# Performance work log

Measured on AMD Instinct MI355X. Metric: run time of the kernel, lower is better.

The kernel has to match this reference:

```python
import jax, jax.numpy as jnp
import numpy as np

BLOCK_SIZE = 16
NVFP4_LEVELS = np.array([0.0, 0.5, 1.0, 1.5, 2.0, 3.0, 4.0, 6.0], dtype=np.float32)


def quantize_to_nvfp4(x, block_size=BLOCK_SIZE):
    """NVFP4 fake-quant: per-16-element block, scale = amax/6, round |x| to nearest level."""
    levels = jnp.asarray(NVFP4_LEVELS, dtype=x.dtype)
    orig_shape = x.shape
    xf = x.reshape(-1, block_size)                                   # [nblk, 16]
    amax = jnp.clip(jnp.max(jnp.abs(xf), axis=-1, keepdims=True), 1e-12)
    scale = amax / 6.0                                               # [nblk, 1]
    x_norm = jnp.abs(xf) / scale                                     # in [0, 6]
    idx = jnp.argmin(jnp.abs(x_norm[..., None] - levels), axis=-1)   # nearest level (first on ties, like torch)
    x_q = jnp.sign(xf) * levels[idx] * scale
    return x_q.reshape(orig_shape)


def _magnitude_mask_2_4(w):
    # keep 2 largest-|.| of every group of 4 along in_features (row-wise 2:4)
    out_f, in_f = w.shape
    a = jnp.abs(w).reshape(out_f, in_f // 4, 4)
    thr = jnp.sort(a, axis=-1)[..., 2:3]          # 2nd-largest magnitude in group
    mask = (a >= thr).reshape(out_f, in_f)
    return mask.astype(w.dtype)


def setup_inputs() -> dict:
    key = jax.random.key(0)
    k_x, k_w, k_s, k_a, k_b, k_bias = jax.random.split(key, 6)
    B, S, IN_F, OUT_F, RANK = 2, 2048, 4096, 4096, 32
    x = jax.random.normal(k_x, (B, S, IN_F), dtype=jnp.float32)
    smooth_scale = jax.random.uniform(k_s, (IN_F,), dtype=jnp.float32, minval=0.5, maxval=2.0)
    # realistic calibrated weight: 2:4 magnitude-sparse then NVFP4 fake-quantized
    w = jax.random.normal(k_w, (OUT_F, IN_F), dtype=jnp.float32) * 0.02
    w_sparse = w * _magnitude_mask_2_4(w)
    w_quantized = quantize_to_nvfp4(w_sparse)
    lora_a = jax.random.normal(k_a, (RANK, IN_F), dtype=jnp.float32) * 0.02
    lora_b = jax.random.normal(k_b, (OUT_F, RANK), dtype=jnp.float32) * 0.02
    bias = jax.random.normal(k_bias, (OUT_F,), dtype=jnp.float32)
    return {"x": x, "smooth_scale": smooth_scale, "w_quantized": w_quantized,
            "lora_a": lora_a, "lora_b": lora_b, "bias": bias}


def reference(x, smooth_scale, w_quantized, lora_a, lora_b, bias):
    # x: [B, S, IN], smooth_scale: [IN], w_quantized: [OUT, IN]
    x_smoothed = x * smooth_scale                                    # SmoothQuant activation scaling
    x_q = quantize_to_nvfp4(x_smoothed, BLOCK_SIZE)                  # block fake-quant of activations
    base_out = jnp.einsum('bsi,oi->bso', x_q, w_quantized)           # 2:4-sparse quantized matmul
    svd_out = jnp.einsum('bsr,or->bso',
                         jnp.einsum('bsi,ri->bsr', x_smoothed, lora_a), lora_b)  # low-rank correction
    return base_out + svd_out + bias
```

## Files before the change

### kernel.cpp

```cpp
#include <hip/hip_runtime.h>
#include <hip/hip_bf16.h>
#include <stdint.h>

typedef __attribute__((ext_vector_type(8)))  __bf16 bf16x8;
typedef __attribute__((ext_vector_type(4)))  float  f32x4;
typedef __attribute__((ext_vector_type(16))) float  f32x16;

#define KP 4160

__device__ inline void async_copy16(const void* g, void* l) {
  __builtin_amdgcn_global_load_lds((const __attribute__((address_space(1))) void*)g,
                                   (__attribute__((address_space(3))) void*)l, 16, 0, 0);
}

__global__ __launch_bounds__(256) void fused_quant_lora_kernel(
    const float* __restrict__ x, const float* __restrict__ ss,
    const float* __restrict__ la, __bf16* __restrict__ Ab,
    float* __restrict__ Tp) {
  __shared__ float red[4][16][32];
  int tid  = threadIdx.x;
  int m0   = blockIdx.x << 4;
  int by   = blockIdx.y;

  {
    int row = m0 + (tid >> 4);
    int cb0 = tid & 15;
#pragma unroll
    for (int i = 0; i < 2; i++) {
      int col = (by << 9) + ((cb0 + (i << 4)) << 4);
      const float4* xp = (const float4*)(x + ((size_t)row << 12) + col);
      const float4* sp = (const float4*)(ss + col);
      float xs[16];
#pragma unroll
      for (int j = 0; j < 4; j++) {
        float4 xv = xp[j]; float4 sv = sp[j];
        xs[4*j+0] = xv.x * sv.x; xs[4*j+1] = xv.y * sv.y;
        xs[4*j+2] = xv.z * sv.z; xs[4*j+3] = xv.w * sv.w;
      }
      float amax = 0.f;
#pragma unroll
      for (int j = 0; j < 16; j++) amax = fmaxf(amax, fabsf(xs[j]));
      amax = fmaxf(amax, 1e-12f);
      float scale = amax / 6.0f;
      bf16x8 o0, o1;
#pragma unroll
      for (int j = 0; j < 16; j++) {
        float a  = fabsf(xs[j]);
        float xn = a / scale;
        float lvl;
        if (xn < 2.25f) {
          lvl = 0.5f * __builtin_ceilf(__builtin_fmaf(2.0f, xn, -0.5f));
        } else {
          lvl = (xn <= 2.5f) ? 2.0f : (xn <= 3.5f) ? 3.0f
              : (xn <= 5.0f) ? 4.0f : 6.0f;
        }
        float mag = lvl * scale;
        float q = (xs[j] > 0.f) ? mag : ((xs[j] < 0.f) ? -mag : 0.f);
        if (j < 8) o0[j] = (__bf16)q; else o1[j-8] = (__bf16)q;
      }
      __bf16* dst = Ab + (size_t)row * KP + col;
      *(bf16x8*)dst = o0;
      *(bf16x8*)(dst + 8) = o1;
    }
  }

  {
    int wave = tid >> 6, lane = tid & 63;
    int lrow = lane & 15, kg = lane >> 4;
    int kbase = (by << 9) + (wave << 7);
    f32x4 acc0 = {0.f,0.f,0.f,0.f}, acc1 = {0.f,0.f,0.f,0.f};
    const float* xrow = x + ((size_t)(m0 + lrow) << 12);
    const float* a0   = la + ((size_t)lrow << 12);
    const float* a1   = a0 + (16 << 12);
#pragma unroll
    for (int k0 = 0; k0 < 128; k0 += 32) {
      int kk = kbase + k0 + (kg << 3);
      float xv[8], sv[8], v0[8], v1[8];
      *(float4*)&xv[0] = *(const float4*)(xrow + kk);
      *(float4*)&xv[4] = *(const float4*)(xrow + kk + 4);
      *(float4*)&sv[0] = *(const float4*)(ss + kk);
      *(float4*)&sv[4] = *(const float4*)(ss + kk + 4);
      *(float4*)&v0[0] = *(const float4*)(a0 + kk);
      *(float4*)&v0[4] = *(const float4*)(a0 + kk + 4);
      *(float4*)&v1[0] = *(const float4*)(a1 + kk);
      *(float4*)&v1[4] = *(const float4*)(a1 + kk + 4);
      bf16x8 af, b0, b1;
#pragma unroll
      for (int j = 0; j < 8; j++) {
        af[j] = (__bf16)(xv[j] * sv[j]);
        b0[j] = (__bf16)v0[j];
        b1[j] = (__bf16)v1[j];
      }
      acc0 = __builtin_amdgcn_mfma_f32_16x16x32_bf16(af, b0, acc0, 0, 0, 0);
      acc1 = __builtin_amdgcn_mfma_f32_16x16x32_bf16(af, b1, acc1, 0, 0, 0);
    }
#pragma unroll
    for (int r = 0; r < 4; r++) {
      red[wave][kg*4 + r][lrow]      = acc0[r];
      red[wave][kg*4 + r][16 + lrow] = acc1[r];
    }
    __syncthreads();
    for (int o = tid; o < 512; o += 256) {
      int rr = o >> 5, cc = o & 31;
      float s = red[0][rr][cc] + red[1][rr][cc] + red[2][rr][cc] + red[3][rr][cc];
      Tp[((size_t)by * 4096 + m0 + rr) * 32 + cc] = s;
    }
  }
}

__global__ __launch_bounds__(256) void wconv_fix_kernel(const float* __restrict__ w,
                                                        const float* __restrict__ lb,
                                                        const float* __restrict__ Tp,
                                                        __bf16* __restrict__ Bb,
                                                        __bf16* __restrict__ Ab) {
  int b = blockIdx.x;
  if (b < 8320) {
    int id  = b * 256 + threadIdx.x;
    int row = id / 520;
    int g   = id - row * 520;
    bf16x8 v;
    if (g < 512) {
      const float4* wp = (const float4*)(w + ((size_t)row << 12) + (g << 3));
      float4 a = wp[0], bb = wp[1];
      v[0]=(__bf16)a.x;  v[1]=(__bf16)a.y;  v[2]=(__bf16)a.z;  v[3]=(__bf16)a.w;
      v[4]=(__bf16)bb.x; v[5]=(__bf16)bb.y; v[6]=(__bf16)bb.z; v[7]=(__bf16)bb.w;
    } else if (g < 516) {
      const float* p = lb + (size_t)row * 32 + ((g - 512) << 3);
#pragma unroll
      for (int j = 0; j < 8; j++) v[j] = (__bf16)p[j];
    } else {
#pragma unroll
      for (int j = 0; j < 8; j++) v[j] = (__bf16)0.f;
    }
    *(bf16x8*)(Bb + (size_t)row * KP + ((size_t)g << 3)) = v;
  } else {
    int id  = (b - 8320) * 256 + threadIdx.x;
    int row = id >> 5, cc = id & 31;
    float s = 0.f;
#pragma unroll
    for (int kc = 0; kc < 8; kc++)
      s += Tp[((size_t)kc * 4096 + row) * 32 + cc];
    __bf16* dst = Ab + (size_t)row * KP + 4096;
    dst[cc]      = (__bf16)s;
    dst[32 + cc] = (__bf16)0.f;
  }
}

#define GBAR() __builtin_amdgcn_s_barrier()
#define PRI1() __builtin_amdgcn_s_setprio(1)
#define PRI0() __builtin_amdgcn_s_setprio(0)
#define WVM(n) asm volatile("s_waitcnt vmcnt(" #n ")" ::: "memory")

#define STG(srcb, dstb, bb, h, t) do {                                         \
    const __bf16* _s = (srcb) + (size_t)(h) * (128 * (size_t)KP)               \
                              + ((size_t)(t) << 6);                            \
    char* _d = (dstb) + ((bb) << 15) + ((h) << 14);                            \
    async_copy16(_s, _d);                                                      \
    async_copy16(_s + 32, _d + 1024);                                          \
  } while (0)

#define KOFF(KS) ((((KS) >> 1) << 10) + ((((KS) & 1) << 5) ^ sx))

#define RD_A(base, KS) do { _Pragma("unroll")                                  \
  for (int mf = 0; mf < 4; mf++)                                               \
    af[mf] = *(const bf16x8*)((base) + (mf << 12) + KOFF(KS)); } while (0)

#define RD_B(base, KS) do {                                                    \
    Br[0*4 + (KS)] = *(const bf16x8*)((base) + KOFF(KS));                      \
    Br[1*4 + (KS)] = *(const bf16x8*)((base) + 4096 + KOFF(KS)); } while (0)

#define MM8(KS) do { _Pragma("unroll")                                         \
  for (int mf = 0; mf < 4; mf++) _Pragma("unroll")                             \
  for (int nf = 0; nf < 2; nf++)                                               \
    acc[mf][nf] = __builtin_amdgcn_mfma_f32_32x32x16_bf16(                     \
        af[mf], Br[nf*4 + (KS)], acc[mf][nf], 0, 0, 0); } while (0)

__global__ __launch_bounds__(512, 2) void gemm_kernel(const __bf16* __restrict__ A,
                                                      const __bf16* __restrict__ B,
                                                      const float* __restrict__ bias,
                                                      float* __restrict__ C) {
  extern __shared__ char lds[];
  const int tid  = threadIdx.x;
  const int w    = tid >> 6, lane = tid & 63;
  const int ln31 = lane & 31, kg2 = lane >> 5;
  const int wm   = w >> 2, wn = w & 3;
  const int bid  = blockIdx.x;
  const int sbid = ((bid & 7) << 5) | (bid >> 3);
  const int bm   = sbid >> 4, bn = sbid & 15;
  const size_t m0 = (size_t)bm << 8, n0 = (size_t)bn << 8;

  const int rr = (w << 4) + (lane >> 2);
  const int kk = ((lane & 3) ^ (((lane >> 5) & 1) << 1) ^ (w & 1)) << 3;
  const __bf16* aS = A + (m0 + rr) * (size_t)KP + kk;
  const __bf16* bS = B + (n0 + rr) * (size_t)KP + kk;
  char* dA = lds + (w << 11);
  char* dB = lds + 65536 + (w << 11);

  const int sx  = (lane & 8) << 2;
  const int k16 = ((kg2 ^ ((ln31 >> 4) & 1)) << 4);
  const int cA = ((ln31 >> 4) << 11) + ((ln31 & 15) << 6) + k16;
  const int cB = ((((wn & 1) << 2) + (ln31 >> 4)) << 11)
               + ((ln31 & 15) << 6) + k16;
  const char* pA0 = lds + (wm << 14) + cA;
  const char* pA1 = pA0 + 32768;
  const char* pB0 = lds + 65536 + ((wn >> 1) << 14) + cB;
  const char* pB1 = pB0 + 32768;

  bf16x8 af[4], Br[8];
  f32x16 acc[4][2];
#pragma unroll
  for (int i = 0; i < 4; i++)
#pragma unroll
    for (int j = 0; j < 2; j++)
#pragma unroll
      for (int q = 0; q < 16; q++) acc[i][j][q] = 0.f;

  STG(bS, dB, 0, 0, 0); STG(bS, dB, 0, 1, 0);
  STG(aS, dA, 0, 0, 0); STG(aS, dA, 0, 1, 0);
  STG(bS, dB, 1, 0, 1); STG(bS, dB, 1, 1, 1);
  WVM(4);
  GBAR();

#pragma unroll 1
  for (int i = 0; i < 32; i++) {
    const int t1 = 2*i + 1, t2 = 2*i + 2;
    int t3 = 2*i + 3; if (t3 > 64) t3 = 64;
    STG(aS, dA, 1, 0, t1);
    RD_B(pB0, 0); RD_B(pB0, 1); RD_A(pA0, 0);
    PRI1(); MM8(0); PRI0();
    GBAR();
    STG(aS, dA, 1, 1, t1);
    RD_B(pB0, 2); RD_B(pB0, 3); RD_A(pA0, 1);
    PRI1(); MM8(1); PRI0();
    GBAR();
    STG(bS, dB, 0, 0, t2);
    RD_A(pA0, 2);
    PRI1(); MM8(2); PRI0();
    GBAR();
    STG(bS, dB, 0, 1, t2);
    RD_A(pA0, 3);
    PRI1(); MM8(3); PRI0();
    WVM(4);
    GBAR();
    STG(aS, dA, 0, 0, t2);
    RD_B(pB1, 0); RD_B(pB1, 1); RD_A(pA1, 0);
    PRI1(); MM8(0); PRI0();
    GBAR();
    STG(aS, dA, 0, 1, t2);
    RD_B(pB1, 2); RD_B(pB1, 3); RD_A(pA1, 1);
    PRI1(); MM8(1); PRI0();
    GBAR();
    STG(bS, dB, 1, 0, t3);
    RD_A(pA1, 2);
    PRI1(); MM8(2); PRI0();
    GBAR();
    STG(bS, dB, 1, 1, t3);
    RD_A(pA1, 3);
    PRI1(); MM8(3); PRI0();
    WVM(4);
    GBAR();
  }

  RD_B(pB0, 0); RD_B(pB0, 1); RD_B(pB0, 2); RD_B(pB0, 3);
  RD_A(pA0, 0); PRI1(); MM8(0); PRI0();
  RD_A(pA0, 1); PRI1(); MM8(1); PRI0();
  RD_A(pA0, 2); PRI1(); MM8(2); PRI0();
  RD_A(pA0, 3); PRI1(); MM8(3); PRI0();

  const int    colb = (int)n0 + (wn << 6) + ln31;
  const size_t rowb = m0 + ((size_t)wm << 7) + (kg2 << 2);
#pragma unroll
  for (int nf = 0; nf < 2; nf++) {
    const int col = colb + (nf << 5);
    const float bv = bias[col];
#pragma unroll
    for (int mf = 0; mf < 4; mf++) {
      const size_t r0 = rowb + ((size_t)mf << 5);
#pragma unroll
      for (int q = 0; q < 16; q++) {
        const size_t row = r0 + (q & 3) + ((q >> 2) << 3);
        C[row * 4096 + col] = acc[mf][nf][q] + bv;
      }
    }
  }
}

extern "C" void kernel_launch(void* const* d_in, const int* in_sizes, int n_in,
                              void* d_out, int out_size, void* d_ws, size_t ws_size,
                              hipStream_t stream) {
  const float* x    = (const float*)d_in[0];
  const float* ss   = (const float*)d_in[1];
  const float* w    = (const float*)d_in[2];
  const float* la   = (const float*)d_in[3];
  const float* lb   = (const float*)d_in[4];
  const float* bias = (const float*)d_in[5];
  float* out = (float*)d_out;

  __bf16* Ab = (__bf16*)d_ws;
  __bf16* Bb = Ab + (size_t)4096 * KP;
  float* Tp = out;

  static bool s_attr = false;
  if (!s_attr) {
    hipFuncSetAttribute((const void*)gemm_kernel,
                        hipFuncAttributeMaxDynamicSharedMemorySize, 131072);
    s_attr = true;
  }

  fused_quant_lora_kernel<<<dim3(256, 8), 256, 0, stream>>>(x, ss, la, Ab, Tp);
  wconv_fix_kernel<<<8832, 256, 0, stream>>>(w, lb, Tp, Bb, Ab);
  gemm_kernel<<<256, 512, 131072, stream>>>(Ab, Bb, bias, out);
}
```

Baseline: 311.9 us.

## Reduce LoRA projection fully in-block and drop partial-sum buffer pass

The quant+LoRA kernel now has each 512-thread block cover the full K dimension for its 16 rows. Its 8 waves each reduce a 512-wide K slice and combine the results in shared memory, then write the rank-32 LoRA activations directly into the bf16 A buffer. This removes the partial-sum buffer (previously parked in the output), its round trip through global memory, and the fix-up blocks in the weight-conversion kernel. The weight conversion is restructured to do two rows per block without a per-thread division. In exchange the grid drops from 2048 to 256 blocks, and each thread carries a longer serial loop.

```diff
diff --git a/kernel.cpp b/kernel.cpp
--- a/kernel.cpp
+++ b/kernel.cpp
@@ -13,21 +13,19 @@
                                    (__attribute__((address_space(3))) void*)l, 16, 0, 0);
 }
 
-__global__ __launch_bounds__(256) void fused_quant_lora_kernel(
+__global__ __launch_bounds__(512) void fused_quant_lora_kernel(
     const float* __restrict__ x, const float* __restrict__ ss,
-    const float* __restrict__ la, __bf16* __restrict__ Ab,
-    float* __restrict__ Tp) {
-  __shared__ float red[4][16][32];
-  int tid  = threadIdx.x;
-  int m0   = blockIdx.x << 4;
-  int by   = blockIdx.y;
+    const float* __restrict__ la, __bf16* __restrict__ Ab) {
+  __shared__ float red[8][16][32];
+  int tid = threadIdx.x;
+  int m0  = blockIdx.x << 4;
 
   {
-    int row = m0 + (tid >> 4);
-    int cb0 = tid & 15;
-#pragma unroll
-    for (int i = 0; i < 2; i++) {
-      int col = (by << 9) + ((cb0 + (i << 4)) << 4);
+    int row = m0 + (tid >> 5);
+    int cb0 = tid & 31;
+#pragma unroll
+    for (int i = 0; i < 8; i++) {
+      int col = (cb0 + (i << 5)) << 4;
       const float4* xp = (const float4*)(x + ((size_t)row << 12) + col);
       const float4* sp = (const float4*)(ss + col);
       float xs[16];
@@ -67,14 +65,13 @@
   {
     int wave = tid >> 6, lane = tid & 63;
     int lrow = lane & 15, kg = lane >> 4;
-    int kbase = (by << 9) + (wave << 7);
     f32x4 acc0 = {0.f,0.f,0.f,0.f}, acc1 = {0.f,0.f,0.f,0.f};
     const float* xrow = x + ((size_t)(m0 + lrow) << 12);
     const float* a0   = la + ((size_t)lrow << 12);
     const float* a1   = a0 + (16 << 12);
-#pragma unroll
-    for (int k0 = 0; k0 < 128; k0 += 32) {
-      int kk = kbase + k0 + (kg << 3);
+#pragma unroll 4
+    for (int k0 = 0; k0 < 16; k0++) {
+      int kk = (wave << 9) + (k0 << 5) + (kg << 3);
       float xv[8], sv[8], v0[8], v1[8];
       *(float4*)&xv[0] = *(const float4*)(xrow + kk);
       *(float4*)&xv[4] = *(const float4*)(xrow + kk + 4);
@@ -100,49 +97,48 @@
       red[wave][kg*4 + r][16 + lrow] = acc1[r];
     }
     __syncthreads();
-    for (int o = tid; o < 512; o += 256) {
-      int rr = o >> 5, cc = o & 31;
-      float s = red[0][rr][cc] + red[1][rr][cc] + red[2][rr][cc] + red[3][rr][cc];
-      Tp[((size_t)by * 4096 + m0 + rr) * 32 + cc] = s;
-    }
-  }
-}
-
-__global__ __launch_bounds__(256) void wconv_fix_kernel(const float* __restrict__ w,
-                                                        const float* __restrict__ lb,
-                                                        const float* __restrict__ Tp,
-                                                        __bf16* __restrict__ Bb,
-                                                        __bf16* __restrict__ Ab) {
-  int b = blockIdx.x;
-  if (b < 8320) {
-    int id  = b * 256 + threadIdx.x;
-    int row = id / 520;
-    int g   = id - row * 520;
-    bf16x8 v;
-    if (g < 512) {
-      const float4* wp = (const float4*)(w + ((size_t)row << 12) + (g << 3));
+    int rr = tid >> 5, cc = tid & 31;
+    float s = 0.f;
+#pragma unroll
+    for (int wv = 0; wv < 8; wv++) s += red[wv][rr][cc];
+    __bf16* dst = Ab + (size_t)(m0 + rr) * KP + 4096;
+    dst[cc]      = (__bf16)s;
+    dst[32 + cc] = (__bf16)0.f;
+  }
+}
+
+__global__ __launch_bounds__(256) void wconv_kernel(const float* __restrict__ w,
+                                                    const float* __restrict__ lb,
+                                                    __bf16* __restrict__ Bb) {
+  int tid = threadIdx.x;
+#pragma unroll
+  for (int r = 0; r < 2; r++) {
+    int row = (blockIdx.x << 1) + r;
+    const float* wr = w + ((size_t)row << 12);
+    __bf16*      br = Bb + (size_t)row * KP;
+#pragma unroll
+    for (int gi = 0; gi < 2; gi++) {
+      int g = tid + (gi << 8);
+      const float4* wp = (const float4*)(wr + (g << 3));
       float4 a = wp[0], bb = wp[1];
+      bf16x8 v;
       v[0]=(__bf16)a.x;  v[1]=(__bf16)a.y;  v[2]=(__bf16)a.z;  v[3]=(__bf16)a.w;
       v[4]=(__bf16)bb.x; v[5]=(__bf16)bb.y; v[6]=(__bf16)bb.z; v[7]=(__bf16)bb.w;
-    } else if (g < 516) {
-      const float* p = lb + (size_t)row * 32 + ((g - 512) << 3);
-#pragma unroll
-      for (int j = 0; j < 8; j++) v[j] = (__bf16)p[j];
-    } else {
-#pragma unroll
-      for (int j = 0; j < 8; j++) v[j] = (__bf16)0.f;
-    }
-    *(bf16x8*)(Bb + (size_t)row * KP + ((size_t)g << 3)) = v;
-  } else {
-    int id  = (b - 8320) * 256 + threadIdx.x;
-    int row = id >> 5, cc = id & 31;
-    float s = 0.f;
-#pragma unroll
-    for (int kc = 0; kc < 8; kc++)
-      s += Tp[((size_t)kc * 4096 + row) * 32 + cc];
-    __bf16* dst = Ab + (size_t)row * KP + 4096;
-    dst[cc]      = (__bf16)s;
-    dst[32 + cc] = (__bf16)0.f;
+      *(bf16x8*)(br + ((size_t)g << 3)) = v;
+    }
+    if (tid < 8) {
+      int g = 512 + tid;
+      bf16x8 v;
+      if (g < 516) {
+        const float* p = lb + (size_t)row * 32 + ((g - 512) << 3);
+#pragma unroll
+        for (int j = 0; j < 8; j++) v[j] = (__bf16)p[j];
+      } else {
+#pragma unroll
+        for (int j = 0; j < 8; j++) v[j] = (__bf16)0.f;
+      }
+      *(bf16x8*)(br + ((size_t)g << 3)) = v;
+    }
   }
 }
 
@@ -298,7 +294,6 @@
 
   __bf16* Ab = (__bf16*)d_ws;
   __bf16* Bb = Ab + (size_t)4096 * KP;
-  float* Tp = out;
 
   static bool s_attr = false;
   if (!s_attr) {
@@ -307,7 +302,7 @@
     s_attr = true;
   }
 
-  fused_quant_lora_kernel<<<dim3(256, 8), 256, 0, stream>>>(x, ss, la, Ab, Tp);
-  wconv_fix_kernel<<<8832, 256, 0, stream>>>(w, lb, Tp, Bb, Ab);
+  fused_quant_lora_kernel<<<256, 512, 0, stream>>>(x, ss, la, Ab);
+  wconv_kernel<<<2048, 256, 0, stream>>>(w, lb, Bb);
   gemm_kernel<<<256, 512, 131072, stream>>>(Ab, Bb, bias, out);
 }
```

Result: no change. 316.9 us (+1.6%).
